# Kernel tuning notes

Measured on AMD Instinct MI355X. Metric: run time of the kernel, lower is better.

Reference implementation:

```python
import jax, jax.numpy as jnp
import numpy as np

H = 2048  # hidden_dim


def setup_inputs() -> dict:
    key = jax.random.key(0)
    ks = jax.random.split(key, 7)
    s = 1.0 / np.sqrt(H)
    x = jax.random.normal(ks[0], (4, 2048, H), dtype=jnp.float32)
    Wq = jax.random.uniform(ks[1], (H, H), jnp.float32, -s, s)
    Wk = jax.random.uniform(ks[2], (H, H), jnp.float32, -s, s)
    Wv = jax.random.uniform(ks[3], (H, H), jnp.float32, -s, s)
    Wo = jax.random.uniform(ks[4], (H, H), jnp.float32, -s, s)
    W1 = jax.random.uniform(ks[5], (H, H), jnp.float32, -s, s)
    W2 = jax.random.uniform(ks[6], (H, H), jnp.float32, -s, s)
    return {"x": x, "Wq": Wq, "Wk": Wk, "Wv": Wv, "Wo": Wo, "W1": W1, "W2": W2}


def reference(x, Wq, Wk, Wv, Wo, W1, W2):
    # Attention (single head, no 1/sqrt(d) scaling, no mask "" faithful to source)
    q = jnp.einsum('bsh,dh->bsd', x, Wq)
    k = jnp.einsum('bsh,dh->bsd', x, Wk)
    v = jnp.einsum('bsh,dh->bsd', x, Wv)
    score = jax.nn.softmax(jnp.einsum('bqd,bkd->bqk', q, k), axis=-1)
    attn = jnp.einsum('bqk,bkd->bqd', score, v)
    attn = jnp.einsum('bsh,dh->bsd', attn, Wo)
    # FFN
    h = jax.nn.relu(jnp.einsum('bsh,dh->bsd', attn, W1))
    y = jnp.einsum('bsh,dh->bsd', h, W2)
    return jnp.sum(y)
```

## Files before the change

kernel.cpp:

```cpp
#include <hip/hip_runtime.h>
#include <hip/hip_bf16.h>
#include <stdint.h>

typedef _Float16 h16_t;
typedef __attribute__((ext_vector_type(8))) _Float16 h16x8;
typedef __attribute__((ext_vector_type(4))) _Float16 h16x4;
typedef __attribute__((ext_vector_type(16))) float f32x16;

static constexpr int HDIM  = 2048;
static constexpr int MROWS = 8192;

__device__ __forceinline__ void gload_lds16(const h16_t* g, h16_t* l) {
  __builtin_amdgcn_global_load_lds(
      (const __attribute__((address_space(1))) void*)g,
      (__attribute__((address_space(3))) void*)l, 16, 0, 0);
}

__device__ __forceinline__ void gemm_core(const h16_t* __restrict__ A,
                                          const h16_t* __restrict__ B,
                                          f32x16 acc[2][2],
                                          h16_t* sA, h16_t* sB) {
  const int tid  = threadIdx.x;
  const int wid  = tid >> 6;
  const int lane = tid & 63;
  const int wr  = (wid >> 1) << 6;
  const int wc  = (wid & 1) << 6;
  const int l31 = lane & 31;
  const int hi  = lane >> 5;
  const int sx  = lane & 7;

#pragma unroll
  for (int i = 0; i < 2; i++)
#pragma unroll
    for (int j = 0; j < 2; j++)
#pragma unroll
      for (int r = 0; r < 16; r++) acc[i][j][r] = 0.0f;

  for (int k0 = 0; k0 < 2048; k0 += 64) {
    __syncthreads();
#pragma unroll
    for (int rnd = 0; rnd < 4; rnd++) {
      const int cid  = rnd * 256 + tid;
      const int row  = cid >> 3;
      const int koct = (cid & 7) ^ (row & 7);
      const long long goff = (long long)row * 2048 + k0 + koct * 8;
      gload_lds16(A + goff, sA + (rnd * 256 + wid * 64) * 8);
      gload_lds16(B + goff, sB + (rnd * 256 + wid * 64) * 8);
    }
    __syncthreads();

#pragma unroll
    for (int ko = 0; ko < 4; ko++) {
      const int po = (2 * ko + hi) ^ sx;
      h16x8 fa[2], fb[2];
#pragma unroll
      for (int i = 0; i < 2; i++)
        fa[i] = *(const h16x8*)(sA + (wr + i * 32 + l31) * 64 + po * 8);
#pragma unroll
      for (int j = 0; j < 2; j++)
        fb[j] = *(const h16x8*)(sB + (wc + j * 32 + l31) * 64 + po * 8);
#pragma unroll
      for (int i = 0; i < 2; i++)
#pragma unroll
        for (int j = 0; j < 2; j++)
          acc[i][j] = __builtin_amdgcn_mfma_f32_32x32x16_f16(
              fa[i], fb[j], acc[i][j], 0, 0, 0);
    }
  }
}

__device__ __forceinline__ void store_c(h16_t* __restrict__ C,
                                        f32x16 acc[2][2], int bm, int bn) {
  const int tid  = threadIdx.x;
  const int wid  = tid >> 6;
  const int lane = tid & 63;
  const int wr = (wid >> 1) << 6, wc = (wid & 1) << 6;
  const int l31 = lane & 31, hi = lane >> 5;
  const int gr = bm * 128 + wr + 4 * hi;
  const int gc = bn * 128 + wc + l31;
#pragma unroll
  for (int i = 0; i < 2; i++)
#pragma unroll
    for (int r = 0; r < 16; r++) {
      const int row = gr + i * 32 + (r & 3) + 8 * (r >> 2);
      const long long ro = (long long)row * 2048;
#pragma unroll
      for (int j = 0; j < 2; j++)
        C[ro + gc + j * 32] = (h16_t)acc[i][j][r];
    }
}

__global__ __launch_bounds__(256)
void gemm_b(const h16_t* __restrict__ Ab, const h16_t* __restrict__ Bb,
            h16_t* __restrict__ Cb, long long sAz, long long sBz, long long sCz)
{
  __shared__ __align__(16) h16_t sA[128 * 64];
  __shared__ __align__(16) h16_t sB[128 * 64];
  const int bn = blockIdx.x, bm = blockIdx.y, z = blockIdx.z;
  const h16_t* A = Ab + (long long)z * sAz + (long long)bm * 128 * 2048;
  const h16_t* B = Bb + (long long)z * sBz + (long long)bn * 128 * 2048;
  f32x16 acc[2][2];
  gemm_core(A, B, acc, sA, sB);
  store_c(Cb + (long long)z * sCz, acc, bm, bn);
}

__global__ __launch_bounds__(256)
void gemm_t_fold(const h16_t* __restrict__ xb, const h16_t* __restrict__ WqkT,
                 h16_t* __restrict__ tb,
                 const h16_t* __restrict__ W1b, const h16_t* __restrict__ GT,
                 h16_t* __restrict__ Wvow)
{
  const int bn = blockIdx.x, bm = blockIdx.y, z = blockIdx.z;
  if (z == 1 && bm >= 16) return;
  __shared__ __align__(16) h16_t sA[128 * 64];
  __shared__ __align__(16) h16_t sB[128 * 64];
  const h16_t* A; const h16_t* B; h16_t* C;
  if (z == 0) { A = xb;  B = WqkT; C = tb; }
  else        { A = W1b; B = GT;   C = Wvow; }
  A += (long long)bm * 128 * 2048;
  B += (long long)bn * 128 * 2048;
  f32x16 acc[2][2];
  gemm_core(A, B, acc, sA, sB);
  store_c(C, acc, bm, bn);
}

__global__ __launch_bounds__(256)
void gemm_ut_softmax(const h16_t* __restrict__ Wvow, const h16_t* __restrict__ xb,
                     h16_t* __restrict__ ut, h16_t* __restrict__ sc)
{
  const int bn = blockIdx.x, bm = blockIdx.y, z = blockIdx.z;
  const int t = threadIdx.x;
  if (z >= 4) {
    const long long row = (long long)(z - 4) * 256 + bm * 16 + bn;
    h16_t* s = sc + row * 2048;
    const int wid = t >> 6, lane = t & 63;
    const h16x8 raw = ((const h16x8*)s)[t];
    float v[8];
    float mx = -3.0e38f;
#pragma unroll
    for (int i = 0; i < 8; i++) { v[i] = (float)raw[i]; mx = fmaxf(mx, v[i]); }
#pragma unroll
    for (int off = 32; off > 0; off >>= 1) mx = fmaxf(mx, __shfl_xor(mx, off, 64));
    __shared__ float sred[4];
    if (lane == 0) sred[wid] = mx;
    __syncthreads();
    mx = fmaxf(fmaxf(sred[0], sred[1]), fmaxf(sred[2], sred[3]));
    float sum = 0.f;
#pragma unroll
    for (int i = 0; i < 8; i++) { v[i] = __expf(v[i] - mx); sum += v[i]; }
#pragma unroll
    for (int off = 32; off > 0; off >>= 1) sum += __shfl_xor(sum, off, 64);
    __syncthreads();
    if (lane == 0) sred[wid] = sum;
    __syncthreads();
    sum = sred[0] + sred[1] + sred[2] + sred[3];
    const float inv = 1.0f / sum;
    h16x8 o;
#pragma unroll
    for (int i = 0; i < 8; i++) o[i] = (h16_t)(v[i] * inv);
    ((h16x8*)s)[t] = o;
    return;
  }
  __shared__ __align__(16) h16_t sA[128 * 64];
  __shared__ __align__(16) h16_t sB[128 * 64];
  const h16_t* A = Wvow + (long long)bm * 128 * 2048;
  const h16_t* B = xb + (long long)z * (long long)MROWS / 4 * 2048 * 2
                      ;
  B = xb + (long long)z * 2048 * 2048 + (long long)bn * 128 * 2048;
  f32x16 acc[2][2];
  gemm_core(A, B, acc, sA, sB);
  store_c(ut + (long long)z * 2048 * 2048, acc, bm, bn);
}

__global__ __launch_bounds__(256)
void gemm_final(const h16_t* __restrict__ P, const h16_t* __restrict__ ut,
                const float* __restrict__ w2p, float* __restrict__ outp)
{
  __shared__ __align__(16) h16_t sA[128 * 64];
  __shared__ __align__(16) h16_t sB[128 * 64];
  const int bn = blockIdx.x, bm = blockIdx.y, z = blockIdx.z;
  const h16_t* A = P  + (long long)z * 2048 * 2048 + (long long)bm * 128 * 2048;
  const h16_t* B = ut + (long long)z * 2048 * 2048 + (long long)bn * 128 * 2048;
  f32x16 acc[2][2];
  gemm_core(A, B, acc, sA, sB);

  const int tid  = threadIdx.x;
  const int wid  = tid >> 6;
  const int lane = tid & 63;
  const int wc = (wid & 1) << 6, l31 = lane & 31;
  const int gc = bn * 128 + wc + l31;
  float w2j[2];
#pragma unroll
  for (int j = 0; j < 2; j++) {
    const int col = gc + j * 32;
    float s = 0.f;
#pragma unroll
    for (int c = 0; c < 16; c++) s += w2p[c * 2048 + col];
    w2j[j] = s;
  }
  float s = 0.f;
#pragma unroll
  for (int i = 0; i < 2; i++)
#pragma unroll
    for (int j = 0; j < 2; j++)
#pragma unroll
      for (int r = 0; r < 16; r++) {
        const float v = acc[i][j][r];
        s += (v > 0.f) ? v * w2j[j] : 0.f;
      }
#pragma unroll
  for (int off = 32; off > 0; off >>= 1) s += __shfl_down(s, off, 64);
  __shared__ float red[4];
  if (lane == 0) red[wid] = s;
  __syncthreads();
  if (tid == 0) atomicAdd(outp, red[0] + red[1] + red[2] + red[3]);
}

__global__ __launch_bounds__(256)
void prologue_kernel(const float* __restrict__ x,  const float* __restrict__ Wq,
                     const float* __restrict__ Wk, const float* __restrict__ Wv,
                     const float* __restrict__ Wo, const float* __restrict__ W1,
                     const float* __restrict__ W2,
                     h16_t* __restrict__ xb,  h16_t* __restrict__ WkT,
                     h16_t* __restrict__ WvT, h16_t* __restrict__ WqT,
                     h16_t* __restrict__ Wob, h16_t* __restrict__ W1b,
                     float* __restrict__ w2p, float* __restrict__ outp)
{
  const int t = threadIdx.x;
  int b = blockIdx.x;
  if (b < 16384) {
    const long long i = (long long)b * 256 + t;
    const float4 v = ((const float4*)x)[i];
    h16x4 o;
    o[0] = (h16_t)v.x; o[1] = (h16_t)v.y; o[2] = (h16_t)v.z; o[3] = (h16_t)v.w;
    ((h16x4*)xb)[i] = o;
    return;
  }
  b -= 16384;
  if (b < 12288) {
    const float* src; h16_t* dst;
    if (b < 4096)      { src = Wk; dst = WkT; }
    else if (b < 8192) { src = Wv; dst = WvT; b -= 4096; }
    else               { src = Wq; dst = WqT; b -= 8192; }
    __shared__ float tl[32][33];
    const int bx = (b & 63) * 32, by = (b >> 6) * 32;
    const int xx = t & 31, y0 = t >> 5;
    for (int y = y0; y < 32; y += 8)
      tl[y][xx] = src[(long long)(by + y) * 2048 + bx + xx];
    __syncthreads();
    for (int y = y0; y < 32; y += 8)
      dst[(long long)(bx + y) * 2048 + by + xx] = (h16_t)tl[xx][y];
    return;
  }
  b -= 12288;
  if (b < 8192) {
    const float* src = (b < 4096) ? Wo : W1;
    h16_t* dst = (b < 4096) ? Wob : W1b;
    const long long i = (long long)(b & 4095) * 256 + t;
    const float4 v = ((const float4*)src)[i];
    h16x4 o;
    o[0] = (h16_t)v.x; o[1] = (h16_t)v.y; o[2] = (h16_t)v.z; o[3] = (h16_t)v.w;
    ((h16x4*)dst)[i] = o;
    return;
  }
  b -= 8192;
  if (b < 128) {
    const int c = b >> 3;
    const int h = (b & 7) * 256 + t;
    float s = 0.f;
#pragma unroll 4
    for (int d = 0; d < 128; d++) s += W2[(long long)(c * 128 + d) * 2048 + h];
    w2p[c * 2048 + h] = s;
    return;
  }
  b -= 128;
  if (b == 0 && t == 0) outp[0] = 0.f;
}

extern "C" void kernel_launch(void* const* d_in, const int* in_sizes, int n_in,
                              void* d_out, int out_size, void* d_ws, size_t ws_size,
                              hipStream_t stream)
{
  const float* x  = (const float*)d_in[0];
  const float* Wq = (const float*)d_in[1];
  const float* Wk = (const float*)d_in[2];
  const float* Wv = (const float*)d_in[3];
  const float* Wo = (const float*)d_in[4];
  const float* W1 = (const float*)d_in[5];
  const float* W2 = (const float*)d_in[6];
  float* out = (float*)d_out;

  const long long HH = (long long)HDIM * HDIM;
  const long long XE = (long long)MROWS * HDIM;

  char* p = (char*)d_ws;
  h16_t* xb   = (h16_t*)p; p += XE * 2;
  h16_t* WkT  = (h16_t*)p; p += HH * 2;
  h16_t* WvT  = (h16_t*)p; p += HH * 2;
  h16_t* WqT  = (h16_t*)p; p += HH * 2;
  h16_t* Wob  = (h16_t*)p; p += HH * 2;
  h16_t* WqkT = (h16_t*)p; p += HH * 2;
  h16_t* GT   = (h16_t*)p; p += HH * 2;
  h16_t* W1b  = (h16_t*)p; p += HH * 2;
  h16_t* Wvow = (h16_t*)p; p += HH * 2;
  h16_t* tb   = (h16_t*)p; p += XE * 2;
  h16_t* sc   = (h16_t*)p; p += XE * 2;
  float* w2p  = (float*)p; p += 16 * HDIM * 4;

  const dim3 b256(256);

  prologue_kernel<<<dim3(16384 + 12288 + 8192 + 128 + 1), b256, 0, stream>>>(
      x, Wq, Wk, Wv, Wo, W1, W2, xb, WkT, WvT, WqT, Wob, W1b, w2p, out);

  gemm_b<<<dim3(16, 16, 2), b256, 0, stream>>>(WkT, WqT, WqkT, HH, HH, HH);

  gemm_t_fold<<<dim3(16, 64, 2), b256, 0, stream>>>(xb, WqkT, tb, W1b, GT, Wvow);

  gemm_b<<<dim3(16, 16, 4), b256, 0, stream>>>(tb, xb, sc, HH, HH, HH);

  gemm_ut_softmax<<<dim3(16, 16, 36), b256, 0, stream>>>(Wvow, xb, tb, sc);

  gemm_final<<<dim3(16, 16, 4), b256, 0, stream>>>(sc, tb, w2p, out);
}
```

Measured before the change: 619.0 us.

## Use 256x256 double-buffered MFMA GEMM core with hand-scheduled LDS pipeline

```diff
diff --git a/kernel.cpp b/kernel.cpp
--- a/kernel.cpp
+++ b/kernel.cpp
@@ -15,6 +15,22 @@
       (const __attribute__((address_space(1))) void*)g,
       (__attribute__((address_space(3))) void*)l, 16, 0, 0);
 }
+
+__device__ __forceinline__ uint32_t ldsaddr(const void* p) {
+  return (uint32_t)(uintptr_t)(const __attribute__((address_space(3))) void*)p;
+}
+
+__device__ __forceinline__ h16x8 dsread(uint32_t off) {
+  h16x8 r;
+  asm volatile("ds_read_b128 %0, %1" : "=v"(r) : "v"(off));
+  return r;
+}
+
+__device__ __forceinline__ void sbar()  { __builtin_amdgcn_sched_barrier(0); }
+__device__ __forceinline__ void bar()   { sbar(); __builtin_amdgcn_s_barrier(); sbar(); }
+__device__ __forceinline__ void waitlg0(){ asm volatile("s_waitcnt lgkmcnt(0)" ::: "memory"); sbar(); }
+__device__ __forceinline__ void waitvm4(){ asm volatile("s_waitcnt vmcnt(4)" ::: "memory"); sbar(); }
+__device__ __forceinline__ void waitvm0(){ asm volatile("s_waitcnt vmcnt(0)" ::: "memory"); sbar(); }
 
 __device__ __forceinline__ void gemm_core(const h16_t* __restrict__ A,
                                           const h16_t* __restrict__ B,
@@ -104,116 +120,230 @@
   store_c(Cb + (long long)z * sCz, acc, bm, bn);
 }
 
-__global__ __launch_bounds__(256)
-void gemm_t_fold(const h16_t* __restrict__ xb, const h16_t* __restrict__ WqkT,
-                 h16_t* __restrict__ tb,
-                 const h16_t* __restrict__ W1b, const h16_t* __restrict__ GT,
-                 h16_t* __restrict__ Wvow)
-{
+__device__ __forceinline__ void core256(const h16_t* __restrict__ A,
+                                        const h16_t* __restrict__ B,
+                                        h16_t* smem, f32x16 acc[4][2])
+{
+  const int tid  = threadIdx.x;
+  const int wid  = tid >> 6, lane = tid & 63;
+  const int wr2  = wid >> 2, wcid = wid & 3;
+  const int l31  = lane & 31, hi = lane >> 5, sx = lane & 7;
+
+  h16_t* pA[2] = { smem,          smem + 32768 };
+  h16_t* pB[2] = { smem + 16384,  smem + 49152 };
+
+  uint32_t poB[4];
+#pragma unroll
+  for (int ks = 0; ks < 4; ks++) poB[ks] = (uint32_t)((((2 * ks + hi) ^ sx) << 4));
+  const uint32_t lrow = (uint32_t)(l31 * 128);
+  uint32_t aT[2], bT[2];
+#pragma unroll
+  for (int b = 0; b < 2; b++) {
+    aT[b] = ldsaddr(pA[b]) + (uint32_t)(wr2 * 128 * 128) + lrow;
+    bT[b] = ldsaddr(pB[b]) + (uint32_t)(wcid * 64 * 128) + lrow;
+  }
+
+  const int srow = tid >> 3;
+  const long long stOff = (long long)srow * HDIM + (long long)(((tid & 7) ^ (srow & 7)) * 8);
+  const int dOff = tid * 8;
+
+  auto stage2 = [&](const h16_t* M, h16_t* panel, int k0, int ci0) {
+#pragma unroll
+    for (int c = 0; c < 2; c++) {
+      const int ci = ci0 + c;
+      gload_lds16(M + stOff + k0 + (long long)ci * (64 * HDIM),
+                  panel + ci * 4096 + dOff);
+    }
+  };
+
+#pragma unroll
+  for (int i = 0; i < 4; i++)
+#pragma unroll
+    for (int j = 0; j < 2; j++)
+#pragma unroll
+      for (int r = 0; r < 16; r++) acc[i][j][r] = 0.0f;
+
+  h16x8 fa0[2][4], fa1[2][4], fb0[4], fb1[4];
+
+  auto rdA = [&](h16x8 (&fa)[2][4], uint32_t base) {
+#pragma unroll
+    for (int mi = 0; mi < 2; mi++)
+#pragma unroll
+      for (int ks = 0; ks < 4; ks++)
+        fa[mi][ks] = dsread(base + (uint32_t)(mi * 32 * 128) + poB[ks]);
+  };
+  auto rdB = [&](h16x8 (&fb)[4], uint32_t base) {
+#pragma unroll
+    for (int ks = 0; ks < 4; ks++) fb[ks] = dsread(base + poB[ks]);
+  };
+  auto mm8 = [&](int am0, int nj, h16x8 (&fa)[2][4], h16x8 (&fb)[4]) {
+#pragma unroll
+    for (int ks = 0; ks < 4; ks++)
+#pragma unroll
+      for (int mi = 0; mi < 2; mi++)
+        acc[am0 + mi][nj] = __builtin_amdgcn_mfma_f32_32x32x16_f16(
+            fa[mi][ks], fb[ks], acc[am0 + mi][nj], 0, 0, 0);
+  };
+
+  auto tile4 = [&](int buf, h16_t* stB, int kB, bool doB,
+                   h16_t* stA, int kA, bool doA, int tailmode) {
+    rdA(fa0, aT[buf]);
+    rdB(fb0, bT[buf]);
+    if (doB) stage2(B, stB, kB, 0);
+    bar(); waitlg0();
+    __builtin_amdgcn_s_setprio(1); mm8(0, 0, fa0, fb0); __builtin_amdgcn_s_setprio(0);
+    bar();
+    rdB(fb1, bT[buf] + 4096);
+    rdA(fa1, aT[buf] + 8192);
+    if (doB) stage2(B, stB, kB, 2);
+    bar(); waitlg0();
+    __builtin_amdgcn_s_setprio(1); mm8(0, 1, fa0, fb1); __builtin_amdgcn_s_setprio(0);
+    bar();
+    if (doA) stage2(A, stA, kA, 0);
+    bar();
+    __builtin_amdgcn_s_setprio(1); mm8(2, 1, fa1, fb1); __builtin_amdgcn_s_setprio(0);
+    bar();
+    if (doA) stage2(A, stA, kA, 2);
+    bar();
+    __builtin_amdgcn_s_setprio(1); mm8(2, 0, fa1, fb0); __builtin_amdgcn_s_setprio(0);
+    if (tailmode == 0) waitvm4(); else if (tailmode == 1) waitvm0();
+    bar();
+  };
+
+  stage2(A, pA[0], 0, 0);  stage2(A, pA[0], 0, 2);
+  stage2(B, pB[0], 0, 0);  stage2(B, pB[0], 0, 2);
+  stage2(A, pA[1], 64, 0); stage2(A, pA[1], 64, 2);
+  waitvm4(); bar();
+
+#pragma unroll 1
+  for (int t = 0; t < 30; t += 2) {
+    tile4(0, pB[1], (t + 1) * 64, true, pA[0], (t + 2) * 64, true, 0);
+    tile4(1, pB[0], (t + 2) * 64, true, pA[1], (t + 3) * 64, true, 0);
+  }
+  tile4(0, pB[1], 31 * 64, true, nullptr, 0, false, 1);
+  tile4(1, nullptr, 0, false, nullptr, 0, false, 2);
+}
+
+__device__ __forceinline__ void store256(h16_t* __restrict__ C,
+                                         f32x16 acc[4][2], int bm, int bn)
+{
+  const int tid = threadIdx.x, wid = tid >> 6, lane = tid & 63;
+  const int wr2 = wid >> 2, wcid = wid & 3;
+  const int l31 = lane & 31, hi = lane >> 5;
+  const int gr0 = bm * 256 + wr2 * 128 + 4 * hi;
+  const int gc0 = bn * 256 + wcid * 64 + l31;
+#pragma unroll
+  for (int am = 0; am < 4; am++)
+#pragma unroll
+    for (int r = 0; r < 16; r++) {
+      const int row = gr0 + am * 32 + (r & 3) + 8 * (r >> 2);
+      const long long ro = (long long)row * HDIM;
+#pragma unroll
+      for (int nj = 0; nj < 2; nj++)
+        C[ro + gc0 + nj * 32] = (h16_t)acc[am][nj][r];
+    }
+}
+
+__global__ __launch_bounds__(512, 2)
+void gemm256_b(const h16_t* __restrict__ Ab, const h16_t* __restrict__ Bb,
+               h16_t* __restrict__ Cb, long long sAz, long long sBz, long long sCz)
+{
+  __shared__ __align__(16) h16_t smem[4 * 16384];
   const int bn = blockIdx.x, bm = blockIdx.y, z = blockIdx.z;
-  if (z == 1 && bm >= 16) return;
-  __shared__ __align__(16) h16_t sA[128 * 64];
-  __shared__ __align__(16) h16_t sB[128 * 64];
-  const h16_t* A; const h16_t* B; h16_t* C;
-  if (z == 0) { A = xb;  B = WqkT; C = tb; }
-  else        { A = W1b; B = GT;   C = Wvow; }
-  A += (long long)bm * 128 * 2048;
-  B += (long long)bn * 128 * 2048;
-  f32x16 acc[2][2];
-  gemm_core(A, B, acc, sA, sB);
-  store_c(C, acc, bm, bn);
-}
-
-__global__ __launch_bounds__(256)
-void gemm_ut_softmax(const h16_t* __restrict__ Wvow, const h16_t* __restrict__ xb,
-                     h16_t* __restrict__ ut, h16_t* __restrict__ sc)
+  const h16_t* A = Ab + (long long)z * sAz + (long long)bm * 256 * HDIM;
+  const h16_t* B = Bb + (long long)z * sBz + (long long)bn * 256 * HDIM;
+  f32x16 acc[4][2];
+  core256(A, B, smem, acc);
+  store256(Cb + (long long)z * sCz, acc, bm, bn);
+}
+
+__global__ __launch_bounds__(512, 2)
+void gemm256_ut_softmax(const h16_t* __restrict__ Wvow, const h16_t* __restrict__ xb,
+                        h16_t* __restrict__ ut, h16_t* __restrict__ sc)
 {
   const int bn = blockIdx.x, bm = blockIdx.y, z = blockIdx.z;
-  const int t = threadIdx.x;
+  const int tid = threadIdx.x;
   if (z >= 4) {
-    const long long row = (long long)(z - 4) * 256 + bm * 16 + bn;
-    h16_t* s = sc + row * 2048;
-    const int wid = t >> 6, lane = t & 63;
-    const h16x8 raw = ((const h16x8*)s)[t];
-    float v[8];
+    const int wid = tid >> 6, lane = tid & 63;
+    const long long row = (long long)(z - 4) * 512 + (bm * 8 + bn) * 8 + wid;
+    h16_t* s = sc + row * HDIM;
+    h16x8 raw[4];
+#pragma unroll
+    for (int i = 0; i < 4; i++) raw[i] = ((const h16x8*)s)[i * 64 + lane];
+    float v[32];
     float mx = -3.0e38f;
 #pragma unroll
-    for (int i = 0; i < 8; i++) { v[i] = (float)raw[i]; mx = fmaxf(mx, v[i]); }
-#pragma unroll
-    for (int off = 32; off > 0; off >>= 1) mx = fmaxf(mx, __shfl_xor(mx, off, 64));
-    __shared__ float sred[4];
-    if (lane == 0) sred[wid] = mx;
-    __syncthreads();
-    mx = fmaxf(fmaxf(sred[0], sred[1]), fmaxf(sred[2], sred[3]));
+    for (int i = 0; i < 32; i++) { v[i] = (float)raw[i >> 3][i & 7]; mx = fmaxf(mx, v[i]); }
+#pragma unroll
+    for (int off = 32; off; off >>= 1) mx = fmaxf(mx, __shfl_xor(mx, off, 64));
     float sum = 0.f;
 #pragma unroll
-    for (int i = 0; i < 8; i++) { v[i] = __expf(v[i] - mx); sum += v[i]; }
-#pragma unroll
-    for (int off = 32; off > 0; off >>= 1) sum += __shfl_xor(sum, off, 64);
-    __syncthreads();
-    if (lane == 0) sred[wid] = sum;
-    __syncthreads();
-    sum = sred[0] + sred[1] + sred[2] + sred[3];
+    for (int i = 0; i < 32; i++) { v[i] = __expf(v[i] - mx); sum += v[i]; }
+#pragma unroll
+    for (int off = 32; off; off >>= 1) sum += __shfl_xor(sum, off, 64);
     const float inv = 1.0f / sum;
-    h16x8 o;
-#pragma unroll
-    for (int i = 0; i < 8; i++) o[i] = (h16_t)(v[i] * inv);
-    ((h16x8*)s)[t] = o;
+#pragma unroll
+    for (int i = 0; i < 4; i++) {
+      h16x8 o;
+#pragma unroll
+      for (int j = 0; j < 8; j++) o[j] = (h16_t)(v[i * 8 + j] * inv);
+      ((h16x8*)s)[i * 64 + lane] = o;
+    }
     return;
   }
-  __shared__ __align__(16) h16_t sA[128 * 64];
-  __shared__ __align__(16) h16_t sB[128 * 64];
-  const h16_t* A = Wvow + (long long)bm * 128 * 2048;
-  const h16_t* B = xb + (long long)z * (long long)MROWS / 4 * 2048 * 2
-                      ;
-  B = xb + (long long)z * 2048 * 2048 + (long long)bn * 128 * 2048;
-  f32x16 acc[2][2];
-  gemm_core(A, B, acc, sA, sB);
-  store_c(ut + (long long)z * 2048 * 2048, acc, bm, bn);
-}
-
-__global__ __launch_bounds__(256)
-void gemm_final(const h16_t* __restrict__ P, const h16_t* __restrict__ ut,
-                const float* __restrict__ w2p, float* __restrict__ outp)
-{
-  __shared__ __align__(16) h16_t sA[128 * 64];
-  __shared__ __align__(16) h16_t sB[128 * 64];
+  __shared__ __align__(16) h16_t smem[4 * 16384];
+  const h16_t* A = Wvow + (long long)bm * 256 * HDIM;
+  const h16_t* B = xb + (long long)z * (long long)HDIM * HDIM + (long long)bn * 256 * HDIM;
+  f32x16 acc[4][2];
+  core256(A, B, smem, acc);
+  store256(ut + (long long)z * (long long)HDIM * HDIM, acc, bm, bn);
+}
+
+__global__ __launch_bounds__(512, 2)
+void gemm256_final(const h16_t* __restrict__ P, const h16_t* __restrict__ utb,
+                   const float* __restrict__ w2p, float* __restrict__ outp)
+{
+  __shared__ __align__(16) h16_t smem[4 * 16384];
   const int bn = blockIdx.x, bm = blockIdx.y, z = blockIdx.z;
-  const h16_t* A = P  + (long long)z * 2048 * 2048 + (long long)bm * 128 * 2048;
-  const h16_t* B = ut + (long long)z * 2048 * 2048 + (long long)bn * 128 * 2048;
-  f32x16 acc[2][2];
-  gemm_core(A, B, acc, sA, sB);
-
-  const int tid  = threadIdx.x;
-  const int wid  = tid >> 6;
-  const int lane = tid & 63;
-  const int wc = (wid & 1) << 6, l31 = lane & 31;
-  const int gc = bn * 128 + wc + l31;
+  const long long HH = (long long)HDIM * HDIM;
+  const h16_t* A = P   + (long long)z * HH + (long long)bm * 256 * HDIM;
+  const h16_t* B = utb + (long long)z * HH + (long long)bn * 256 * HDIM;
+  f32x16 acc[4][2];
+  core256(A, B, smem, acc);
+
+  const int tid = threadIdx.x, wid = tid >> 6, lane = tid & 63;
+  const int wcid = wid & 3, l31 = lane & 31;
+  const int gc0 = bn * 256 + wcid * 64 + l31;
   float w2j[2];
 #pragma unroll
-  for (int j = 0; j < 2; j++) {
-    const int col = gc + j * 32;
+  for (int nj = 0; nj < 2; nj++) {
+    const int col = gc0 + nj * 32;
     float s = 0.f;
 #pragma unroll
-    for (int c = 0; c < 16; c++) s += w2p[c * 2048 + col];
-    w2j[j] = s;
+    for (int c = 0; c < 16; c++) s += w2p[c * HDIM + col];
+    w2j[nj] = s;
   }
   float s = 0.f;
 #pragma unroll
-  for (int i = 0; i < 2; i++)
-#pragma unroll
-    for (int j = 0; j < 2; j++)
+  for (int am = 0; am < 4; am++)
+#pragma unroll
+    for (int nj = 0; nj < 2; nj++)
 #pragma unroll
       for (int r = 0; r < 16; r++) {
-        const float v = acc[i][j][r];
-        s += (v > 0.f) ? v * w2j[j] : 0.f;
+        const float vv = acc[am][nj][r];
+        s += (vv > 0.f) ? vv * w2j[nj] : 0.f;
       }
 #pragma unroll
-  for (int off = 32; off > 0; off >>= 1) s += __shfl_down(s, off, 64);
-  __shared__ float red[4];
+  for (int off = 32; off; off >>= 1) s += __shfl_down(s, off, 64);
+  __shared__ float red[8];
   if (lane == 0) red[wid] = s;
   __syncthreads();
-  if (tid == 0) atomicAdd(outp, red[0] + red[1] + red[2] + red[3]);
+  if (tid == 0) {
+    float t = 0.f;
+#pragma unroll
+    for (int w = 0; w < 8; w++) t += red[w];
+    atomicAdd(outp, t);
+  }
 }
 
 __global__ __launch_bounds__(256)
@@ -307,18 +437,20 @@
   h16_t* sc   = (h16_t*)p; p += XE * 2;
   float* w2p  = (float*)p; p += 16 * HDIM * 4;
 
-  const dim3 b256(256);
+  const dim3 b256(256), b512(512);
 
   prologue_kernel<<<dim3(16384 + 12288 + 8192 + 128 + 1), b256, 0, stream>>>(
       x, Wq, Wk, Wv, Wo, W1, W2, xb, WkT, WvT, WqT, Wob, W1b, w2p, out);
 
   gemm_b<<<dim3(16, 16, 2), b256, 0, stream>>>(WkT, WqT, WqkT, HH, HH, HH);
 
-  gemm_t_fold<<<dim3(16, 64, 2), b256, 0, stream>>>(xb, WqkT, tb, W1b, GT, Wvow);
-
-  gemm_b<<<dim3(16, 16, 4), b256, 0, stream>>>(tb, xb, sc, HH, HH, HH);
-
-  gemm_ut_softmax<<<dim3(16, 16, 36), b256, 0, stream>>>(Wvow, xb, tb, sc);
-
-  gemm_final<<<dim3(16, 16, 4), b256, 0, stream>>>(sc, tb, w2p, out);
-}
+  gemm_b<<<dim3(16, 16, 1), b256, 0, stream>>>(W1b, GT, Wvow, 0, 0, 0);
+
+  gemm256_b<<<dim3(8, 32, 1), b512, 0, stream>>>(xb, WqkT, tb, 0, 0, 0);
+
+  gemm256_b<<<dim3(8, 8, 4), b512, 0, stream>>>(tb, xb, sc, HH, HH, HH);
+
+  gemm256_ut_softmax<<<dim3(8, 8, 20), b512, 0, stream>>>(Wvow, xb, tb, sc);
+
+  gemm256_final<<<dim3(8, 8, 4), b512, 0, stream>>>(sc, tb, w2p, out);
+}
```

New measurement: 1.176 ms. 90.0% more time.
